# Kernel optimization log

Measured on AMD Instinct MI355X. Metric: run time of the kernel, lower is better.

Reference implementation:

```python
import jax, jax.numpy as jnp
import numpy as np

E = 2          # n_modalities
HQ = 16        # n_heads
HK = 8         # n_kv_heads
HD = 128       # head_dim
DIM = 2048
BS = 2
SEQ = 2048
EPS = 1e-6
ROPE_THETA = 10000.0


def _rmsnorm(x, w):
    # x: (..., d), w broadcastable to x
    return x * jax.lax.rsqrt(jnp.mean(x * x, axis=-1, keepdims=True) + EPS) * w


def _apply_rope(t, cos, sin):
    # t: (bs, seq, H, HD); cos/sin: (seq, HD//2). Complex rotation on pairs.
    t2 = t.reshape(*t.shape[:-1], HD // 2, 2)
    t0, t1 = t2[..., 0], t2[..., 1]
    c = cos[None, :, None, :]
    s = sin[None, :, None, :]
    out = jnp.stack([t0 * c - t1 * s, t0 * s + t1 * c], axis=-1)
    return out.reshape(t.shape)


def setup_inputs() -> dict:
    key = jax.random.key(0)
    ks = jax.random.split(key, 8)
    pos = jnp.arange(SEQ, dtype=jnp.float32)
    inv_freq = 1.0 / (ROPE_THETA ** (jnp.arange(0, HD, 2, dtype=jnp.float32) / HD))
    ang = pos[:, None] * inv_freq[None, :]  # (SEQ, HD//2)
    return {
        "x": jax.random.normal(ks[0], (BS, SEQ, DIM), jnp.float32),
        "freqs_cos": jnp.cos(ang),
        "freqs_sin": jnp.sin(ang),
        "wq": jax.random.normal(ks[1], (E, DIM, HQ * HD), jnp.float32) * 0.02,
        "wk": jax.random.normal(ks[2], (E, DIM, HK * HD), jnp.float32) * 0.02,
        "wv": jax.random.normal(ks[3], (E, DIM, HK * HD), jnp.float32) * 0.02,
        "wo": jax.random.normal(ks[4], (E, HQ * HD, DIM), jnp.float32) * 0.02,
        "q_norm_w": jnp.ones((E, HD), jnp.float32),
        "k_norm_w": jnp.ones((E, HD), jnp.float32),
        "attn_norm_w": jnp.ones((E, DIM), jnp.float32),
        "modality_ids": jax.random.randint(ks[5], (BS * SEQ,), 0, E, jnp.int32),
    }


def reference(x, freqs_cos, freqs_sin, wq, wk, wv, wo,
              q_norm_w, k_norm_w, attn_norm_w, modality_ids):
    bs, seq, dim = x.shape
    xf = x.reshape(-1, dim)  # (N, dim)
    onehot = (modality_ids[None, :] == jnp.arange(E, dtype=modality_ids.dtype)[:, None]).astype(x.dtype)  # (E, N)

    # Per-modality QKV projections + QK RMSNorm, then combine by modality id
    q = jnp.einsum('nd,edh->enh', xf, wq).reshape(E, -1, HQ, HD)
    q = _rmsnorm(q, q_norm_w[:, None, None, :])
    q = jnp.einsum('en,enhd->nhd', onehot, q).reshape(bs, seq, HQ, HD)

    k = jnp.einsum('nd,edh->enh', xf, wk).reshape(E, -1, HK, HD)
    k = _rmsnorm(k, k_norm_w[:, None, None, :])
    k = jnp.einsum('en,enhd->nhd', onehot, k).reshape(bs, seq, HK, HD)

    v = jnp.einsum('nd,edh->enh', xf, wv).reshape(E, -1, HK, HD)
    v = jnp.einsum('en,enhd->nhd', onehot, v).reshape(bs, seq, HK, HD)

    # RoPE
    q = _apply_rope(q, freqs_cos, freqs_sin)
    k = _apply_rope(k, freqs_cos, freqs_sin)

    # repeat_kv for GQA
    n_rep = HQ // HK
    k = jnp.repeat(k, n_rep, axis=2)
    v = jnp.repeat(v, n_rep, axis=2)

    # Global causal SDPA
    qh = jnp.swapaxes(q, 1, 2)  # (bs, HQ, seq, HD)
    kh = jnp.swapaxes(k, 1, 2)
    vh = jnp.swapaxes(v, 1, 2)
    scores = jnp.einsum('bhqd,bhkd->bhqk', qh, kh) / jnp.sqrt(jnp.asarray(HD, x.dtype))
    causal = jnp.tril(jnp.ones((seq, seq), dtype=bool))
    scores = jnp.where(causal[None, None], scores, jnp.asarray(-1e30, x.dtype))
    attn = jax.nn.softmax(scores, axis=-1)
    out = jnp.einsum('bhqk,bhkd->bhqd', attn, vh)
    out_flat = jnp.swapaxes(out, 1, 2).reshape(-1, HQ * HD)  # (N, HQ*HD)

    # Per-modality output projection + RMSNorm, combine
    o = jnp.einsum('nh,ehd->end', out_flat, wo)  # (E, N, dim)
    o = _rmsnorm(o, attn_norm_w[:, None, :])
    o = jnp.einsum('en,end->nd', onehot, o)
    return o.reshape(bs, seq, dim)
```

## Files before the change

### kernel.cpp

```cpp
#include <hip/hip_runtime.h>

#define E_ 2
#define HQ_ 16
#define HK_ 8
#define HD_ 128
#define DIM_ 2048
#define BS_ 2
#define SEQ_ 2048
#define NTOK 4096

typedef unsigned short ushort_t;
typedef short bf16x8 __attribute__((ext_vector_type(8)));
typedef unsigned short ushort8 __attribute__((ext_vector_type(8)));
typedef float f32x4 __attribute__((ext_vector_type(4)));

#define MFMA(a, b, c) __builtin_amdgcn_mfma_f32_16x16x32_bf16(a, b, c, 0, 0, 0)

__device__ __forceinline__ unsigned short f2bf(float f) {
  unsigned u = __builtin_bit_cast(unsigned, f);
  u = (u + 0x7FFFu + ((u >> 16) & 1u)) >> 16;
  return (unsigned short)u;
}
__device__ __forceinline__ float bf2f(unsigned short h) {
  unsigned u = ((unsigned)h) << 16;
  return __builtin_bit_cast(float, u);
}

__device__ __forceinline__ void glds16(const void* g, void* s) {
  __builtin_amdgcn_global_load_lds(
      (const __attribute__((address_space(1))) unsigned int*)g,
      (__attribute__((address_space(3))) unsigned int*)s, 16, 0, 0);
}

__global__ __launch_bounds__(1024) void build_crow(const int* __restrict__ ids,
                                                   int* __restrict__ cnt, int* __restrict__ crow) {
  __shared__ int sc[1024];
  __shared__ int total0;
  const int t = threadIdx.x;
  int id4[4];
  int c = 0;
  for (int j = 0; j < 4; j++) {
    id4[j] = ids[t * 4 + j];
    c += (id4[j] == 0);
  }
  sc[t] = c;
  __syncthreads();
  for (int off = 1; off < 1024; off <<= 1) {
    int v = sc[t];
    int add = (t >= off) ? sc[t - off] : 0;
    __syncthreads();
    sc[t] = v + add;
    __syncthreads();
  }
  if (t == 1023) total0 = sc[1023];
  __syncthreads();
  const int cnt0 = total0;
  if (t == 0) {
    cnt[0] = cnt0;
    cnt[1] = NTOK - cnt0;
  }
  int p0 = sc[t] - c;
  int r0 = 0;
  for (int j = 0; j < 4; j++) {
    int n = t * 4 + j;
    int cr;
    if (id4[j] == 0) {
      cr = p0 + r0;
      r0++;
    } else {
      cr = cnt0 + (n - (p0 + r0));
    }
    crow[n] = cr;
  }
}

__global__ __launch_bounds__(256) void convert_scatter(const float* __restrict__ x,
                                                       const int* __restrict__ crow,
                                                       ushort_t* __restrict__ xb) {
  const int token = blockIdx.x;
  const int cr = crow[token];
  const long src = (long)token * DIM_ + threadIdx.x * 8;
  const long dst = (long)cr * DIM_ + threadIdx.x * 8;
  float4 a = *(const float4*)(x + src);
  float4 b = *(const float4*)(x + src + 4);
  ushort8 o;
  o[0] = f2bf(a.x); o[1] = f2bf(a.y); o[2] = f2bf(a.z); o[3] = f2bf(a.w);
  o[4] = f2bf(b.x); o[5] = f2bf(b.y); o[6] = f2bf(b.z); o[7] = f2bf(b.w);
  *(ushort8*)(xb + dst) = o;
}

__global__ __launch_bounds__(256) void transpose_w3(const float* __restrict__ wq,
                                                    const float* __restrict__ wk,
                                                    const float* __restrict__ wv,
                                                    ushort_t* __restrict__ out) {
  __shared__ float tile[32][33];
  const int e = blockIdx.z;
  const int xx = blockIdx.x;
  const float* inp;
  int N, outBase, n0;
  if (xx < 64) {
    inp = wq + (long)e * 2048 * 2048; N = 2048; outBase = 0;    n0 = xx * 32;
  } else if (xx < 96) {
    inp = wk + (long)e * 2048 * 1024; N = 1024; outBase = 2048; n0 = (xx - 64) * 32;
  } else {
    inp = wv + (long)e * 2048 * 1024; N = 1024; outBase = 3072; n0 = (xx - 96) * 32;
  }
  ushort_t* outp = out + (long)e * 4096 * 2048;
  const int k0 = blockIdx.y * 32;
  const int tx = threadIdx.x & 31, ty = threadIdx.x >> 5;
  for (int i = 0; i < 4; i++)
    tile[ty + i * 8][tx] = inp[(long)(k0 + ty + i * 8) * N + n0 + tx];
  __syncthreads();
  for (int i = 0; i < 4; i++)
    outp[(long)(outBase + n0 + ty + i * 8) * 2048 + k0 + tx] = f2bf(tile[tx][ty + i * 8]);
}

__global__ __launch_bounds__(256) void transpose_f2b(const float* __restrict__ in,
                                                     ushort_t* __restrict__ out, int K, int N,
                                                     long inE, long outE, int outBase) {
  __shared__ float tile[32][33];
  int e = blockIdx.z;
  const float* inp = in + (long)e * inE;
  ushort_t* outp = out + (long)e * outE;
  int n0 = blockIdx.x * 32, k0 = blockIdx.y * 32;
  int tx = threadIdx.x & 31, ty = threadIdx.x >> 5;
  for (int i = 0; i < 4; i++)
    tile[ty + i * 8][tx] = inp[(long)(k0 + ty + i * 8) * N + n0 + tx];
  __syncthreads();
  for (int i = 0; i < 4; i++)
    outp[(long)(outBase + n0 + ty + i * 8) * K + k0 + tx] = f2bf(tile[tx][ty + i * 8]);
}

__global__ __launch_bounds__(256) void transpose_v(const ushort_t* __restrict__ qkv,
                                                   const int* __restrict__ crow,
                                                   ushort_t* __restrict__ vt) {
  __shared__ ushort_t tile[32][34];
  int z = blockIdx.z;
  int b = z / HK_, hk = z % HK_;
  int s0 = blockIdx.x * 32, d0 = blockIdx.y * 32;
  int tx = threadIdx.x & 31, ty = threadIdx.x >> 5;
  for (int i = 0; i < 4; i++) {
    int cr = crow[b * SEQ_ + s0 + ty + i * 8];
    tile[ty + i * 8][tx] = qkv[(long)cr * 4096 + 3072 + hk * 128 + d0 + tx];
  }
  __syncthreads();
  for (int i = 0; i < 4; i++)
    vt[((long)(b * HK_ + hk) * 128 + d0 + ty + i * 8) * SEQ_ + s0 + tx] = tile[tx][ty + i * 8];
}

__global__ __launch_bounds__(256, 3) void gemm_bt_slot(const ushort_t* __restrict__ A,
                                                       const ushort_t* __restrict__ BT,
                                                       ushort_t* __restrict__ C, int K, int Nc,
                                                       const int* __restrict__ cnt, long btE) {
  __shared__ __align__(16) char lds[49152];
  const int cnt0 = cnt[0];
  const int nA = (cnt0 + 127) >> 7;
  const int slot = blockIdx.y, bn = blockIdx.x;
  const int e = (slot < nA) ? 0 : 1;
  const int bm = e ? slot - nA : slot;
  const int scnt = e ? (NTOK - cnt0) : cnt0;
  if (bm * 128 >= scnt) return;
  const int sbase = e ? cnt0 : 0;
  const ushort_t* Bte = BT + (long)e * btE;

  const int t = threadIdx.x, w = t >> 6, lane = t & 63;
  const int quad = lane >> 4, l16 = lane & 15;
  const int wr = w >> 1, wc = w & 1;

  const int arow0 = sbase + bm * 128;
  const int brow0 = bn * 128;

  const int srow = t >> 2;
  const int lc = ((t & 3) - (srow >> 1)) & 3;
  int ga1 = arow0 + srow;       if (ga1 > NTOK - 1) ga1 = NTOK - 1;
  int ga2 = arow0 + 64 + srow;  if (ga2 > NTOK - 1) ga2 = NTOK - 1;
  const ushort_t* sA1 = A + (long)ga1 * K + lc * 8;
  const ushort_t* sA2 = A + (long)ga2 * K + lc * 8;
  const ushort_t* sB1 = Bte + (long)(brow0 + srow) * K + lc * 8;
  const ushort_t* sB2 = Bte + (long)(brow0 + 64 + srow) * K + lc * 8;

  f32x4 acc[4][4];
#pragma unroll
  for (int i = 0; i < 4; i++)
#pragma unroll
    for (int j = 0; j < 4; j++) acc[i][j] = (f32x4){0.f, 0.f, 0.f, 0.f};

#define STAGE(ps, kk)                                \
  glds16(sA1 + (kk), (ps) + w * 1024);               \
  glds16(sA2 + (kk), (ps) + 4096 + w * 1024);        \
  glds16(sB1 + (kk), (ps) + 8192 + w * 1024);        \
  glds16(sB2 + (kk), (ps) + 12288 + w * 1024);

  char* pr = lds;
  char* pn = lds + 16384;
  char* p2 = lds + 32768;

  STAGE(pr, 0);
  STAGE(pn, 32);
  asm volatile("s_waitcnt vmcnt(4)" ::: "memory");
  __builtin_amdgcn_s_barrier();

  const int NT = K >> 5;
  for (int kt = 0; kt < NT; kt++) {
    const bool st = (kt + 2) < NT;
    if (st) { STAGE(p2, (kt + 2) * 32); }
    bf16x8 af[4], bfv[4];
#pragma unroll
    for (int mf = 0; mf < 4; mf++) {
      const int lr = wr * 64 + mf * 16 + l16;
      af[mf] = *(const bf16x8*)(pr + lr * 64 + ((quad + (lr >> 1)) & 3) * 16);
    }
#pragma unroll
    for (int nf = 0; nf < 4; nf++) {
      const int c = wc * 64 + nf * 16 + l16;
      bfv[nf] = *(const bf16x8*)(pr + 8192 + c * 64 + ((quad + (c >> 1)) & 3) * 16);
    }
    asm volatile("s_waitcnt lgkmcnt(0)" ::: "memory");
    __builtin_amdgcn_sched_barrier(0);
    __builtin_amdgcn_s_setprio(1);
#pragma unroll
    for (int mf = 0; mf < 4; mf++)
#pragma unroll
      for (int nf = 0; nf < 4; nf++) acc[mf][nf] = MFMA(af[mf], bfv[nf], acc[mf][nf]);
    __builtin_amdgcn_s_setprio(0);
    if (st) asm volatile("s_waitcnt vmcnt(4)" ::: "memory");
    else    asm volatile("s_waitcnt vmcnt(0)" ::: "memory");
    __builtin_amdgcn_s_barrier();
    char* tmp = pr; pr = pn; pn = p2; p2 = tmp;
  }
#undef STAGE

#pragma unroll
  for (int mf = 0; mf < 4; mf++) {
#pragma unroll
    for (int reg = 0; reg < 4; reg++) {
      const int rl = wr * 64 + mf * 16 + quad * 4 + reg;
      if (bm * 128 + rl >= scnt) continue;
      ushort_t* Cp = C + (long)(arow0 + rl) * Nc + brow0 + wc * 64 + l16;
#pragma unroll
      for (int nf = 0; nf < 4; nf++) Cp[nf * 16] = f2bf(acc[mf][nf][reg]);
    }
  }
}

__global__ __launch_bounds__(256) void fuse_rmsrope(
    const ushort_t* __restrict__ qkv, const int* __restrict__ crow, const float* __restrict__ qw,
    const float* __restrict__ kw, const float* __restrict__ fc, const float* __restrict__ fs,
    const int* __restrict__ ids, ushort_t* __restrict__ qout, ushort_t* __restrict__ kout) {
  const int token = blockIdx.x;
  const int slot = blockIdx.y * 4 + (threadIdx.x >> 6);
  const int lane = threadIdx.x & 63;
  const int b = token >> 11, s = token & 2047;
  const int e = ids[token];
  const int cr = crow[token];
  const bool isq = slot < 16;
  const int h = isq ? slot : slot - 16;
  const ushort_t* src = qkv + (long)cr * 4096 + (isq ? slot * 128 : 2048 + h * 128);
  unsigned pv = *(const unsigned*)(src + 2 * lane);
  float v0 = bf2f((unsigned short)pv), v1 = bf2f((unsigned short)(pv >> 16));
  float ss = v0 * v0 + v1 * v1;
  ss += __shfl_xor(ss, 32); ss += __shfl_xor(ss, 16); ss += __shfl_xor(ss, 8);
  ss += __shfl_xor(ss, 4);  ss += __shfl_xor(ss, 2);  ss += __shfl_xor(ss, 1);
  float r = rsqrtf(ss * (1.0f / 128.0f) + 1e-6f);
  const float* nw = (isq ? qw : kw) + e * 128;
  v0 *= r * nw[2 * lane];
  v1 *= r * nw[2 * lane + 1];
  float c = fc[s * 64 + lane], sn = fs[s * 64 + lane];
  float o0 = v0 * c - v1 * sn;
  float o1 = v0 * sn + v1 * c;
  ushort_t* dst;
  if (isq) {
    const float QS = 0.08838834764831845f * 1.4426950408889634f;
    o0 *= QS; o1 *= QS;
    dst = qout + ((long)(b * HQ_ + h) * SEQ_ + s) * 128;
  } else {
    dst = kout + ((long)(b * HK_ + h) * SEQ_ + s) * 128;
  }
  *(unsigned*)(dst + 2 * lane) = (unsigned)f2bf(o0) | ((unsigned)f2bf(o1) << 16);
}

__global__ __launch_bounds__(256, 2) void attn_kernel(const ushort_t* __restrict__ Q,
                                                      const ushort_t* __restrict__ K,
                                                      const ushort_t* __restrict__ VT,
                                                      const int* __restrict__ crow,
                                                      ushort_t* __restrict__ O) {
  __shared__ __align__(16) ushort_t Ks[2][64 * 128];
  __shared__ __align__(16) ushort_t Vs[2][128 * 64];
  __shared__ __align__(16) ushort_t Ps[4][16][72];

  const int bh = blockIdx.y;
  const int b = bh >> 4, h = bh & 15, hk = h >> 1;
  const int t = threadIdx.x, w = t >> 6, lane = t & 63;
  const int quad = lane >> 4, l16 = lane & 15;

  const ushort_t* qbase = Q + ((long)(b * HQ_ + h) * SEQ_) * HD_;
  const ushort_t* kbase = K + ((long)(b * HK_ + hk) * SEQ_) * HD_;
  const ushort_t* vtbase = VT + ((long)(b * HK_ + hk) * HD_) * SEQ_;

#define STAGEKV(bi, s0)                                                                     \
  for (int c = 0; c < 4; c++) {                                                             \
    int lin = c * 4096 + w * 1024 + lane * 16;                                              \
    int row = lin >> 8;                                                                     \
    int gc = (((lin >> 4) & 15) - row) & 15;                                                \
    glds16(kbase + (long)((s0) + row) * HD_ + gc * 8, (char*)Ks[bi] + c * 4096 + w * 1024); \
    int d = lin >> 7;                                                                       \
    int gc2 = (((lin >> 4) & 7) - d) & 7;                                                   \
    glds16(vtbase + (long)d * SEQ_ + (s0) + gc2 * 8, (char*)Vs[bi] + c * 4096 + w * 1024);  \
  }

  const f32x4 zero = {0.f, 0.f, 0.f, 0.f};

  for (int half = 0; half < 2; half++) {
    const int qi = half ? (int)blockIdx.x : 31 - (int)blockIdx.x;
    const int q0 = qi * 64;

    for (int c = 0; c < 4; c++) {
      int lin = c * 4096 + w * 1024 + lane * 16;
      int row = lin >> 8;
      int gc = (((lin >> 4) & 15) - row) & 15;
      glds16(qbase + (long)(q0 + row) * HD_ + gc * 8, (char*)Ks[0] + c * 4096 + w * 1024);
    }
    __syncthreads();
    bf16x8 qf[4];
    {
      int row = w * 16 + l16;
      for (int kk = 0; kk < 4; kk++) {
        int cl = (kk * 4 + quad + row) & 15;
        qf[kk] = *(const bf16x8*)((const char*)Ks[0] + row * 256 + cl * 16);
      }
    }
    __syncthreads();

    f32x4 oa[8];
    for (int i = 0; i < 8; i++) oa[i] = zero;
    float rs[4] = {0.f, 0.f, 0.f, 0.f};

    const int nkt = qi + 1;
    STAGEKV(0, 0);
    __syncthreads();
    int buf = 0;
    for (int kt = 0; kt < nkt; kt++) {
      const int s0 = kt * 64;
      if (kt + 1 < nkt) STAGEKV(buf ^ 1, s0 + 64);
      const char* Kb = (const char*)Ks[buf];
      const char* Vb = (const char*)Vs[buf];

      f32x4 sa[4];
      __builtin_amdgcn_s_setprio(1);
      for (int cb = 0; cb < 4; cb++) {
        sa[cb] = zero;
        int n = cb * 16 + l16;
        for (int kk = 0; kk < 4; kk++) {
          int cl = (kk * 4 + quad + n) & 15;
          bf16x8 kfrag = *(const bf16x8*)(Kb + n * 256 + cl * 16);
          sa[cb] = MFMA(qf[kk], kfrag, sa[cb]);
        }
      }
      __builtin_amdgcn_s_setprio(0);
      if (kt == nkt - 1) {
        for (int cb = 0; cb < 4; cb++)
          for (int r = 0; r < 4; r++)
            if (cb * 16 + l16 > q0 + w * 16 + quad * 4 + r - s0) sa[cb][r] = -1e30f;
      }
      for (int cb = 0; cb < 4; cb++)
        for (int r = 0; r < 4; r++) {
          float p = exp2f(sa[cb][r]);
          rs[r] += p;
          Ps[w][quad * 4 + r][cb * 16 + l16] = f2bf(p);
        }
      __builtin_amdgcn_s_setprio(1);
      for (int kk2 = 0; kk2 < 2; kk2++) {
        bf16x8 pf = *(const bf16x8*)&Ps[w][l16][kk2 * 32 + quad * 8];
        for (int vb = 0; vb < 8; vb++) {
          int d = vb * 16 + l16;
          int cl = (kk2 * 4 + quad + d) & 7;
          bf16x8 vfrag = *(const bf16x8*)(Vb + d * 128 + cl * 16);
          oa[vb] = MFMA(pf, vfrag, oa[vb]);
        }
      }
      __builtin_amdgcn_s_setprio(0);
      __syncthreads();
      buf ^= 1;
    }

    float inv[4];
    int cr4[4];
    for (int r = 0; r < 4; r++) {
      float v = rs[r];
      v += __shfl_xor(v, 1);
      v += __shfl_xor(v, 2);
      v += __shfl_xor(v, 4);
      v += __shfl_xor(v, 8);
      inv[r] = 1.0f / v;
      cr4[r] = crow[b * SEQ_ + q0 + w * 16 + quad * 4 + r];
    }
    for (int vb = 0; vb < 8; vb++)
      for (int r = 0; r < 4; r++) {
        long off = (long)cr4[r] * 2048 + h * 128 + vb * 16 + l16;
        O[off] = f2bf(oa[vb][r] * inv[r]);
      }
  }
#undef STAGEKV
}

__global__ __launch_bounds__(256) void out_rmsnorm(const ushort_t* __restrict__ o_raw,
                                                   const int* __restrict__ crow,
                                                   const float* __restrict__ wn,
                                                   const int* __restrict__ ids,
                                                   float* __restrict__ out) {
  __shared__ float red[4];
  const int token = blockIdx.x;
  const int t = threadIdx.x, w = t >> 6, lane = t & 63;
  const int e = ids[token];
  const int cr = crow[token];
  ushort8 u = *(const ushort8*)(o_raw + (long)cr * 2048 + t * 8);
  float v[8];
  float ss = 0.f;
  for (int j = 0; j < 8; j++) {
    v[j] = bf2f(u[j]);
    ss += v[j] * v[j];
  }
  ss += __shfl_xor(ss, 32); ss += __shfl_xor(ss, 16); ss += __shfl_xor(ss, 8);
  ss += __shfl_xor(ss, 4);  ss += __shfl_xor(ss, 2);  ss += __shfl_xor(ss, 1);
  if (lane == 0) red[w] = ss;
  __syncthreads();
  float tot = red[0] + red[1] + red[2] + red[3];
  float r = rsqrtf(tot * (1.0f / 2048.0f) + 1e-6f);
  const float* wp = wn + (long)e * 2048 + t * 8;
  float* op = out + (long)token * 2048 + t * 8;
  for (int j = 0; j < 8; j++) op[j] = v[j] * r * wp[j];
}

extern "C" void kernel_launch(void* const* d_in, const int* in_sizes, int n_in, void* d_out,
                              int out_size, void* d_ws, size_t ws_size, hipStream_t stream) {
  const float* x = (const float*)d_in[0];
  const float* fc = (const float*)d_in[1];
  const float* fs = (const float*)d_in[2];
  const float* wq = (const float*)d_in[3];
  const float* wk = (const float*)d_in[4];
  const float* wv = (const float*)d_in[5];
  const float* wo = (const float*)d_in[6];
  const float* qnw = (const float*)d_in[7];
  const float* knw = (const float*)d_in[8];
  const float* anw = (const float*)d_in[9];
  const int* ids = (const int*)d_in[10];
  float* out = (float*)d_out;
  char* ws = (char*)d_ws;

  ushort_t* x_bf = (ushort_t*)(ws + 0);
  ushort_t* wqkvT = (ushort_t*)(ws + (16l << 20));
  ushort_t* woT = (ushort_t*)(ws + (16l << 20));
  int* cnt = (int*)(ws + (48l << 20));
  int* crow = (int*)(ws + (48l << 20) + 64);
  ushort_t* qkvraw = (ushort_t*)(ws + (64l << 20));
  ushort_t* qfh = (ushort_t*)(ws + (96l << 20));
  ushort_t* kfh = (ushort_t*)(ws + (112l << 20));
  ushort_t* vt = (ushort_t*)(ws + (120l << 20));
  ushort_t* o_flat = x_bf;
  ushort_t* o_raw = qkvraw;

  build_crow<<<1, 1024, 0, stream>>>(ids, cnt, crow);
  convert_scatter<<<NTOK, 256, 0, stream>>>(x, crow, x_bf);
  transpose_w3<<<dim3(128, 64, E_), 256, 0, stream>>>(wq, wk, wv, wqkvT);
  gemm_bt_slot<<<dim3(32, 33), 256, 0, stream>>>(x_bf, wqkvT, qkvraw, 2048, 4096, cnt,
                                                 (long)4096 * 2048);
  transpose_f2b<<<dim3(64, 64, E_), 256, 0, stream>>>(wo, woT, 2048, 2048, (long)2048 * 2048,
                                                      (long)2048 * 2048, 0);
  fuse_rmsrope<<<dim3(NTOK, 6), 256, 0, stream>>>(qkvraw, crow, qnw, knw, fc, fs, ids, qfh, kfh);
  transpose_v<<<dim3(64, 4, BS_ * HK_), 256, 0, stream>>>(qkvraw, crow, vt);
  attn_kernel<<<dim3(16, 32), 256, 0, stream>>>(qfh, kfh, vt, crow, o_flat);
  gemm_bt_slot<<<dim3(16, 33), 256, 0, stream>>>(o_flat, woT, o_raw, 2048, 2048, cnt,
                                                 (long)2048 * 2048);
  out_rmsnorm<<<NTOK, 256, 0, stream>>>(o_raw, crow, anw, ids, out);
}
```

Measured before the change: 431.7 us.

## Use 256x128-tile 512-thread GEMM with triple-buffered LDS for QKV projection

Adds a new GEMM kernel with 256-row tiles, 8 waves and a three-stage LDS ring buffer, and uses it for the QKV projection instead of the 128-row slot kernel. Tiles are laid over the sorted token order. A tile that straddles the modality boundary computes against both weight sets and keeps only the rows belonging to each. The aim is more reuse of each B tile per block, fewer launched blocks and deeper load/compute overlap. The cost is that the one boundary tile does twice the work, and the larger LDS and register footprint may limit occupancy.

Result: slower. 465.8 us (+7.9%).

```diff
diff --git a/kernel.cpp b/kernel.cpp
--- a/kernel.cpp
+++ b/kernel.cpp
@@ -146,6 +146,123 @@
   __syncthreads();
   for (int i = 0; i < 4; i++)
     vt[((long)(b * HK_ + hk) * 128 + d0 + ty + i * 8) * SEQ_ + s0 + tx] = tile[tx][ty + i * 8];
+}
+
+__global__ __launch_bounds__(512, 4) void gemm_bt_big(const ushort_t* __restrict__ A,
+                                                      const ushort_t* __restrict__ BT,
+                                                      ushort_t* __restrict__ C, int K, int Nc,
+                                                      const int* __restrict__ cnt, long btE) {
+  __shared__ __align__(16) char lds[73728];
+  const int cnt0 = cnt[0];
+  const int bn = blockIdx.x, slot = blockIdx.y;
+  const int row0 = slot * 256;
+
+  const int t = threadIdx.x, w = t >> 6, lane = t & 63;
+  const int quad = lane >> 4, l16 = lane & 15;
+  const int wr = w >> 2, wc = w & 3;
+  const int brow0 = bn * 128;
+
+  const int srow = t >> 2;
+  const int lc = ((t & 3) - (srow >> 1)) & 3;
+  const ushort_t* sA0 = A + (long)(row0 + srow) * K + lc * 8;
+  const ushort_t* sA1 = A + (long)(row0 + 128 + srow) * K + lc * 8;
+
+#define STAGE(ps, kk)                           \
+  glds16(sA0 + (kk), (ps) + w * 1024);          \
+  glds16(sA1 + (kk), (ps) + 8192 + w * 1024);   \
+  glds16(sB0 + (kk), (ps) + 16384 + w * 1024);
+
+#define KLOOP(ACC)                                                                        \
+  {                                                                                       \
+    char* pr = lds;                                                                       \
+    char* pn = lds + 24576;                                                               \
+    char* p2 = lds + 49152;                                                               \
+    STAGE(pr, 0);                                                                         \
+    STAGE(pn, 32);                                                                        \
+    asm volatile("s_waitcnt vmcnt(3)" ::: "memory");                                      \
+    __builtin_amdgcn_s_barrier();                                                         \
+    const int NT = K >> 5;                                                                \
+    for (int kt = 0; kt < NT; kt++) {                                                     \
+      const bool st = (kt + 2) < NT;                                                      \
+      if (st) { STAGE(p2, (kt + 2) * 32); }                                               \
+      bf16x8 af[8], bfv[2];                                                               \
+      _Pragma("unroll") for (int mf = 0; mf < 8; mf++) {                                  \
+        const int lr = mf * 16 + l16;                                                     \
+        af[mf] = *(const bf16x8*)(pr + wr * 8192 + lr * 64 + ((quad + (lr >> 1)) & 3) * 16); \
+      }                                                                                   \
+      _Pragma("unroll") for (int nf = 0; nf < 2; nf++) {                                  \
+        const int c = wc * 32 + nf * 16 + l16;                                            \
+        bfv[nf] = *(const bf16x8*)(pr + 16384 + c * 64 + ((quad + (c >> 1)) & 3) * 16);   \
+      }                                                                                   \
+      asm volatile("s_waitcnt lgkmcnt(0)" ::: "memory");                                  \
+      __builtin_amdgcn_sched_barrier(0);                                                  \
+      __builtin_amdgcn_s_setprio(1);                                                      \
+      _Pragma("unroll") for (int mf = 0; mf < 8; mf++) {                                  \
+        ACC[mf][0] = MFMA(af[mf], bfv[0], ACC[mf][0]);                                    \
+        ACC[mf][1] = MFMA(af[mf], bfv[1], ACC[mf][1]);                                    \
+      }                                                                                   \
+      __builtin_amdgcn_s_setprio(0);                                                      \
+      if (st) asm volatile("s_waitcnt vmcnt(3)" ::: "memory");                            \
+      else    asm volatile("s_waitcnt vmcnt(0)" ::: "memory");                            \
+      __builtin_amdgcn_s_barrier();                                                       \
+      char* tmp = pr; pr = pn; pn = p2; p2 = tmp;                                         \
+    }                                                                                     \
+  }
+
+  const bool pure = (row0 + 256 <= cnt0) || (row0 >= cnt0);
+  if (pure) {
+    const int e0 = (row0 >= cnt0) ? 1 : 0;
+    const ushort_t* Bte = BT + (long)e0 * btE;
+    const ushort_t* sB0 = Bte + (long)(brow0 + srow) * K + lc * 8;
+
+    f32x4 acc[8][2];
+#pragma unroll
+    for (int i = 0; i < 8; i++) {
+      acc[i][0] = (f32x4){0.f, 0.f, 0.f, 0.f};
+      acc[i][1] = (f32x4){0.f, 0.f, 0.f, 0.f};
+    }
+    KLOOP(acc);
+
+#pragma unroll
+    for (int mf = 0; mf < 8; mf++) {
+#pragma unroll
+      for (int reg = 0; reg < 4; reg++) {
+        const int grow = row0 + wr * 128 + mf * 16 + quad * 4 + reg;
+        ushort_t* Cp = C + (long)grow * Nc + brow0 + wc * 32 + l16;
+        Cp[0] = f2bf(acc[mf][0][reg]);
+        Cp[16] = f2bf(acc[mf][1][reg]);
+      }
+    }
+  } else {
+    for (int ee = 0; ee < 2; ee++) {
+      const ushort_t* Bte = BT + (long)ee * btE;
+      const ushort_t* sB0 = Bte + (long)(brow0 + srow) * K + lc * 8;
+
+      f32x4 acc[8][2];
+#pragma unroll
+      for (int i = 0; i < 8; i++) {
+        acc[i][0] = (f32x4){0.f, 0.f, 0.f, 0.f};
+        acc[i][1] = (f32x4){0.f, 0.f, 0.f, 0.f};
+      }
+      KLOOP(acc);
+
+#pragma unroll
+      for (int mf = 0; mf < 8; mf++) {
+#pragma unroll
+        for (int reg = 0; reg < 4; reg++) {
+          const int grow = row0 + wr * 128 + mf * 16 + quad * 4 + reg;
+          const bool mine = ee ? (grow >= cnt0) : (grow < cnt0);
+          if (!mine) continue;
+          ushort_t* Cp = C + (long)grow * Nc + brow0 + wc * 32 + l16;
+          Cp[0] = f2bf(acc[mf][0][reg]);
+          Cp[16] = f2bf(acc[mf][1][reg]);
+        }
+      }
+      __syncthreads();
+    }
+  }
+#undef KLOOP
+#undef STAGE
 }
 
 __global__ __launch_bounds__(256, 3) void gemm_bt_slot(const ushort_t* __restrict__ A,
@@ -462,8 +579,8 @@
   build_crow<<<1, 1024, 0, stream>>>(ids, cnt, crow);
   convert_scatter<<<NTOK, 256, 0, stream>>>(x, crow, x_bf);
   transpose_w3<<<dim3(128, 64, E_), 256, 0, stream>>>(wq, wk, wv, wqkvT);
-  gemm_bt_slot<<<dim3(32, 33), 256, 0, stream>>>(x_bf, wqkvT, qkvraw, 2048, 4096, cnt,
-                                                 (long)4096 * 2048);
+  gemm_bt_big<<<dim3(32, 16), 512, 0, stream>>>(x_bf, wqkvT, qkvraw, 2048, 4096, cnt,
+                                                (long)4096 * 2048);
   transpose_f2b<<<dim3(64, 64, E_), 256, 0, stream>>>(wo, woT, 2048, 2048, (long)2048 * 2048,
                                                       (long)2048 * 2048, 0);
   fuse_rmsrope<<<dim3(NTOK, 6), 256, 0, stream>>>(qkvraw, crow, qnw, knw, fc, fs, ids, qfh, kfh);
```
